# Kernel tuning notes

Hardware: AMD Instinct MI355X
Metric: run time of the kernel (lower is better)

Reference implementation:

```python
import jax, jax.numpy as jnp
import numpy as np

B, C, H, W = 8, 192, 64, 64
HEADS = 4


def _conv(x, w, groups=1):
    # NCHW conv, stride 1, SAME padding (matches 1x1 pad=0 and 3x3 pad=1)
    return jax.lax.conv_general_dilated(
        x, w, window_strides=(1, 1), padding='SAME',
        dimension_numbers=('NCHW', 'OIHW', 'NCHW'),
        feature_group_count=groups)


def setup_inputs() -> dict:
    key = jax.random.key(0)
    k1, k2, k3, k4 = jax.random.split(key, 4)
    x = jax.random.normal(k1, (B, C, H, W), dtype=jnp.float32)
    y = jax.random.normal(k2, (B, C, H, W), dtype=jnp.float32)
    # qkv: Conv2d(C, 3C, 1, bias=False) -> weight (3C, C, 1, 1)
    w_qkv = jax.random.normal(k3, (3 * C, C, 1, 1), dtype=jnp.float32) * 0.02
    # qkv_conv: depthwise Conv2d(3C, 3C, 3, padding=1, groups=3C) -> weight (3C, 1, 3, 3)
    w_dw = jax.random.normal(k4, (3 * C, 1, 3, 3), dtype=jnp.float32) * 0.1
    temperature = jnp.ones((1, HEADS, 1, 1), dtype=jnp.float32)
    return {'x': x, 'y': y, 'w_qkv': w_qkv, 'w_dw': w_dw, 'temperature': temperature}


def reference(x, y, w_qkv, w_dw, temperature):
    b, c, h, w = x.shape
    hw = h * w
    dh = c // HEADS

    def qkv(t):
        t = _conv(_conv(t, w_qkv), w_dw, groups=3 * c)  # (b, 3c, h, w)
        q, k, v = jnp.split(t, 3, axis=1)
        rs = lambda a: a.reshape(b, HEADS, dh, hw)
        return rs(q), rs(k), rs(v)

    q, k, v = qkv(x)
    q1, k1, v1 = qkv(y)

    # F.normalize along last dim (eps = 1e-12)
    def nrm(a):
        n = jnp.sqrt(jnp.sum(a * a, axis=-1, keepdims=True))
        return a / jnp.maximum(n, 1e-12)

    q, k, q1, k1 = nrm(q), nrm(k), nrm(q1), nrm(k1)

    # channel attention: (b, heads, dh, dh), temperature broadcasts (1, heads, 1, 1)
    attn = lambda a, bk: jax.nn.softmax(
        jnp.einsum('bhcn,bhdn->bhcd', a, bk) * temperature, axis=-1)

    attn_u = attn(q, k)
    attn_ud = attn(q, k1)
    attn_d = attn(q1, k1)
    attn_du = attn(q1, k)

    mm = lambda A, V: jnp.einsum('bhcd,bhdn->bhcn', A, V)
    cross_feature = (mm(attn_du, v) + mm(attn_ud, v1)).reshape(b, c, h, w)
    self_feature = (mm(attn_u, v) + mm(attn_d, v1)).reshape(b, c, h, w)
    return cross_feature, self_feature
```

## Files before the change

### kernel.cpp

```cpp
#include <hip/hip_runtime.h>

#define CC   192
#define C3   576
#define HH   64
#define WW   64
#define HWP  4096
#define BB   8
#define DH   48
#define QKV_B (C3*HWP)
#define X_B   (CC*HWP)
#define OUT_HALF ((size_t)BB*X_B)

typedef short bf16x8 __attribute__((ext_vector_type(8)));
typedef float f32x4  __attribute__((ext_vector_type(4)));

#define AS1(p) ((__attribute__((address_space(1))) void*)(p))
#define AS3(p) ((__attribute__((address_space(3))) void*)(p))

__device__ __forceinline__ ushort f2bf(float v) {
    union { float f; unsigned u; } a; a.f = v;
    unsigned r = a.u + 0x7FFF + ((a.u >> 16) & 1);
    return (ushort)(r >> 16);
}
__device__ __forceinline__ float bf2f(ushort h) {
    union { float f; unsigned u; } a; a.u = ((unsigned)h) << 16; return a.f;
}

__global__ __launch_bounds__(256) void convert_single_kernel(const float* __restrict__ in,
    ushort* __restrict__ xt)
{
    __shared__ float L[64][65];
    const int n0 = blockIdx.x * 64, c0 = blockIdx.y * 64, b = blockIdx.z;
    const int t = threadIdx.x;
    const float* ip = in + (size_t)b * X_B;
    #pragma unroll
    for (int i = 0; i < 16; i++) {
        int e = t + 256 * i;
        int r = e >> 6, col = e & 63;
        L[r][col] = ip[(size_t)(c0 + r) * HWP + n0 + col];
    }
    __syncthreads();
    #pragma unroll
    for (int i = 0; i < 4; i++) {
        int e = t + 256 * i;
        int n = e >> 4, c4 = e & 15;
        ushort hi[4];
        #pragma unroll
        for (int j = 0; j < 4; j++)
            hi[j] = f2bf(L[c4 * 4 + j][n]);
        size_t base = ((size_t)(b * HWP + n0 + n)) * 192 + c0 + c4 * 4;
        *(ushort4*)&xt[base] = make_ushort4(hi[0], hi[1], hi[2], hi[3]);
    }
}

__global__ __launch_bounds__(256) void vtrans_kernel(const ushort* __restrict__ in,
    ushort* __restrict__ vt)
{
    __shared__ __align__(16) ushort L[64][72];
    const int n0 = blockIdx.x * 64, c0 = blockIdx.y * 64, b = blockIdx.z;
    const int t = threadIdx.x;
    const ushort* ip = in + (size_t)b * X_B;
    #pragma unroll
    for (int i = 0; i < 2; i++) {
        int e = t + 256 * i;
        int r = e >> 3, u8 = e & 7;
        *(bf16x8*)&L[r][u8 * 8] = *(const bf16x8*)&ip[(size_t)(c0 + r) * HWP + n0 + u8 * 8];
    }
    __syncthreads();
    #pragma unroll
    for (int i = 0; i < 4; i++) {
        int e = t + 256 * i;
        int n = e >> 4, c4 = e & 15;
        ushort o[4];
        #pragma unroll
        for (int j = 0; j < 4; j++) o[j] = L[c4 * 4 + j][n];
        *(ushort4*)&vt[((size_t)(b * HWP + n0 + n)) * 192 + c0 + c4 * 4] =
            make_ushort4(o[0], o[1], o[2], o[3]);
    }
}

__global__ __launch_bounds__(256) void wconvert_kernel(const float* __restrict__ wq,
    ushort* __restrict__ wc)
{
    int e = (blockIdx.x * 256 + threadIdx.x) * 4;
    int oc = e / 192, k = e % 192;
    ushort o[4] = {0, 0, 0, 0};
    if (oc < C3) {
        #pragma unroll
        for (int j = 0; j < 4; j++)
            o[j] = f2bf(wq[oc * CC + k + j]);
    }
    *(ushort4*)&wc[e] = make_ushort4(o[0], o[1], o[2], o[3]);
}

__global__ __launch_bounds__(256) void conv1x1_mfma(const ushort* __restrict__ XT,
    const ushort* __restrict__ Wc, ushort* __restrict__ t1s)
{
    __shared__ __align__(16) ushort Sall[4][128 * 32];
    const int t = threadIdx.x;
    const int lane = t & 63, w = t >> 6;
    const int wm = w >> 1, wn = w & 1;
    const int fr = lane & 15, kg = lane >> 4;
    const int g = blockIdx.x;
    const int xcd = g & 7, s = g >> 3;
    const int bg = xcd;
    const int nt = s / 5;
    const int mi = s % 5;
    const int n0 = nt * 128;
    const int m0 = mi * 128;

    f32x4 acc[4][4] = {};

    auto STAGE = [&](int buf, int ck) {
        const int k0 = ck * 32;
        #pragma unroll
        for (int i = 0; i < 2; i++) {
            int u = i * 256 + w * 64 + lane;
            int rp = u >> 3;
            int p = (u & 7) ^ (rp & 7);
            int r = (rp << 1) | (p >> 2);
            int c = p & 3;
            const ushort* gwh = Wc + (size_t)(m0 + r) * 192 + k0 + c * 8;
            __builtin_amdgcn_global_load_lds(AS1(gwh), AS3(&Sall[buf][(i * 256 + w * 64) * 8]), 16, 0, 0);
            const ushort* gx = XT + ((size_t)(bg * HWP + n0 + r)) * 192 + k0 + c * 8;
            __builtin_amdgcn_global_load_lds(AS1(gx), AS3(&Sall[2 + buf][(i * 256 + w * 64) * 8]), 16, 0, 0);
        }
    };

    STAGE(0, 0);
    __syncthreads();
    int cur = 0;
    for (int ck = 0; ck < 6; ck++) {
        if (ck < 5) STAGE(cur ^ 1, ck + 1);
        bf16x8 afh[4], bfr[4];
        #pragma unroll
        for (int m = 0; m < 4; m++) {
            int R = wm * 64 + m * 16 + fr;
            int unit = (R >> 1) * 8 + ((((R & 1) << 2) | kg) ^ ((R >> 1) & 7));
            afh[m] = *(const bf16x8*)&Sall[cur][unit * 8];
        }
        #pragma unroll
        for (int n = 0; n < 4; n++) {
            int R = wn * 64 + n * 16 + fr;
            int unit = (R >> 1) * 8 + ((((R & 1) << 2) | kg) ^ ((R >> 1) & 7));
            bfr[n] = *(const bf16x8*)&Sall[2 + cur][unit * 8];
        }
        #pragma unroll
        for (int m = 0; m < 4; m++)
            #pragma unroll
            for (int n = 0; n < 4; n++)
                acc[m][n] = __builtin_amdgcn_mfma_f32_16x16x32_bf16(afh[m], bfr[n], acc[m][n], 0, 0, 0);
        __syncthreads();
        cur ^= 1;
    }

    ushort (*E)[128] = (ushort(*)[128])Sall;
    #pragma unroll
    for (int m = 0; m < 4; m++) {
        int rl = wm * 64 + m * 16 + kg * 4;
        #pragma unroll
        for (int n = 0; n < 4; n++) {
            int cl = wn * 64 + n * 16 + fr;
            #pragma unroll
            for (int r = 0; r < 4; r++)
                E[rl + r][cl] = f2bf(acc[m][n][r]);
        }
    }
    __syncthreads();
    ushort* ob = t1s + (size_t)bg * QKV_B;
    #pragma unroll
    for (int i = 0; i < 8; i++) {
        int u = t + 256 * i;
        int row = u >> 4, c8 = u & 15;
        int oc = m0 + row;
        if (oc < C3)
            *(bf16x8*)&ob[(size_t)oc * HWP + n0 + c8 * 8] = *(bf16x8*)&E[row][c8 * 8];
    }
}

__global__ __launch_bounds__(256) void dw3x3_kernel(const ushort* __restrict__ inp,
    const float* __restrict__ wd,
    ushort* __restrict__ qh, ushort* __restrict__ vv, float* __restrict__ inv)
{
    __shared__ float P[66][72];
    const int bc = blockIdx.x;
    const int b = bc / C3, ch = bc % C3;
    const int t = threadIdx.x;
    const ushort* ip = inp + (size_t)bc * HWP;
    float wr[9];
    #pragma unroll
    for (int k = 0; k < 9; k++) wr[k] = wd[ch * 9 + k];
    for (int i = t; i < 66 * 72; i += 256) ((float*)P)[i] = 0.f;
    __syncthreads();
    #pragma unroll
    for (int i = 0; i < 2; i++) {
        int u = t + 256 * i;
        int y = u >> 3, x0 = (u & 7) * 8;
        bf16x8 v8 = *(const bf16x8*)&ip[u * 8];
        #pragma unroll
        for (int j = 0; j < 8; j++)
            P[1 + y][4 + x0 + j] = bf2f((ushort)v8[j]);
    }
    __syncthreads();

    float ssum = 0.f;
    #pragma unroll
    for (int i = 0; i < 4; i++) {
        int u = t + 256 * i;
        int y0 = u >> 4;
        int x0 = (u & 15) * 4;
        float res[4] = {0.f, 0.f, 0.f, 0.f};
        #pragma unroll
        for (int dy = 0; dy < 3; dy++) {
            float4 A = *(float4*)&P[y0 + dy][x0];
            float4 Bv = *(float4*)&P[y0 + dy][x0 + 4];
            float4 Cv = *(float4*)&P[y0 + dy][x0 + 8];
            float c0 = A.w, c1 = Bv.x, c2 = Bv.y, c3 = Bv.z, c4 = Bv.w, c5 = Cv.x;
            float w0 = wr[dy*3], w1 = wr[dy*3+1], w2 = wr[dy*3+2];
            res[0] += w0*c0 + w1*c1 + w2*c2;
            res[1] += w0*c1 + w1*c2 + w2*c3;
            res[2] += w0*c2 + w1*c3 + w2*c4;
            res[3] += w0*c3 + w1*c4 + w2*c5;
        }
        #pragma unroll
        for (int k = 0; k < 4; k++) ssum += res[k] * res[k];
        if (ch < 384) {
            size_t base = ((size_t)b * 384 + ch) * HWP + u * 4;
            *(ushort4*)&qh[base] = make_ushort4(f2bf(res[0]), f2bf(res[1]),
                                                f2bf(res[2]), f2bf(res[3]));
        } else {
            size_t base = ((size_t)b * CC + (ch - 384)) * HWP + u * 4;
            *(ushort4*)&vv[base] = make_ushort4(f2bf(res[0]), f2bf(res[1]),
                                                f2bf(res[2]), f2bf(res[3]));
        }
    }
    if (ch < 384) {
        #pragma unroll
        for (int off = 32; off > 0; off >>= 1) ssum += __shfl_down(ssum, off);
        __shared__ float red[4];
        if ((t & 63) == 0) red[t >> 6] = ssum;
        __syncthreads();
        if (t == 0) {
            float tot = red[0] + red[1] + red[2] + red[3];
            inv[b * 384 + ch] = 1.f / fmaxf(sqrtf(tot), 1e-12f);
        }
    }
}

__global__ __launch_bounds__(256) void gram_mfma(const ushort* __restrict__ qhx,
    const ushort* __restrict__ qhy, float* __restrict__ spart)
{
    __shared__ __align__(16) ushort As[96 * 64];
    __shared__ __align__(16) ushort Bs[96 * 64];
    const int chunk = blockIdx.x, bh = blockIdx.y;
    const int b = bh >> 2, h = bh & 3;
    const int t = threadIdx.x;
    const int lane = t & 63, w = t >> 6;
    const int wm = w >> 1, wn = w & 1;
    const int fr = lane & 15, kg = lane >> 4;

    const size_t qbase = ((size_t)b * 384 + h * DH) * HWP;
    const size_t kbase = ((size_t)b * 384 + 192 + h * DH) * HWP;

    f32x4 acc[3][3] = {};

    for (int ks = 0; ks < 8; ks++) {
        const int n0 = chunk * 512 + ks * 64;
        #pragma unroll
        for (int i = 0; i < 3; i++) {
            int u = i * 256 + w * 64 + lane;
            int r = u >> 3, c = u & 7;
            int cs = c ^ (r & 7);
            const ushort* ga = ((r < DH) ? (qhx + qbase + (size_t)r * HWP)
                                         : (qhy + qbase + (size_t)(r - DH) * HWP))
                               + n0 + cs * 8;
            __builtin_amdgcn_global_load_lds(AS1(ga), AS3(&As[(size_t)(i * 4 + w) * 512]), 16, 0, 0);
            const ushort* gb = ((r < DH) ? (qhx + kbase + (size_t)r * HWP)
                                         : (qhy + kbase + (size_t)(r - DH) * HWP))
                               + n0 + cs * 8;
            __builtin_amdgcn_global_load_lds(AS1(gb), AS3(&Bs[(size_t)(i * 4 + w) * 512]), 16, 0, 0);
        }
        __syncthreads();
        #pragma unroll
        for (int kq = 0; kq < 8; kq += 4) {
            bf16x8 af[3], bfr[3];
            #pragma unroll
            for (int m = 0; m < 3; m++) {
                int R = wm * DH + m * 16 + fr;
                int unit = R * 8 + ((kq + kg) ^ (R & 7));
                af[m] = *(const bf16x8*)&As[unit * 8];
            }
            #pragma unroll
            for (int n = 0; n < 3; n++) {
                int R = wn * DH + n * 16 + fr;
                int unit = R * 8 + ((kq + kg) ^ (R & 7));
                bfr[n] = *(const bf16x8*)&Bs[unit * 8];
            }
            #pragma unroll
            for (int m = 0; m < 3; m++)
                #pragma unroll
                for (int n = 0; n < 3; n++)
                    acc[m][n] = __builtin_amdgcn_mfma_f32_16x16x32_bf16(af[m], bfr[n], acc[m][n], 0, 0, 0);
        }
        __syncthreads();
    }

    float* sp = spart + ((size_t)chunk * 32 + bh) * 9216;
    #pragma unroll
    for (int m = 0; m < 3; m++) {
        int row = wm * DH + m * 16 + kg * 4;
        #pragma unroll
        for (int n = 0; n < 3; n++) {
            int col = wn * DH + n * 16 + fr;
            #pragma unroll
            for (int r = 0; r < 4; r++)
                sp[(row + r) * 96 + col] = acc[m][n][r];
        }
    }
}

__global__ __launch_bounds__(256) void softmax_kernel(const float* __restrict__ spart,
    const float* __restrict__ invx, const float* __restrict__ invy,
    const float* __restrict__ temp, ushort* __restrict__ mpp)
{
    __shared__ float G[96][97];
    const int bh = blockIdx.x, b = bh >> 2, h = bh & 3;
    const int t = threadIdx.x;
    const float ts = temp[h];
    for (int i = 0; i < 36; i++) {
        int f = t + 256 * i;
        float s = 0.f;
        #pragma unroll
        for (int cch = 0; cch < 8; cch++)
            s += spart[((size_t)cch * 32 + bh) * 9216 + f];
        int r = f / 96, c = f % 96;
        float iq = (r < DH) ? invx[b*384 + h*DH + r] : invy[b*384 + h*DH + (r-DH)];
        float ik = (c < DH) ? invx[b*384 + CC + h*DH + c] : invy[b*384 + CC + h*DH + (c-DH)];
        G[r][c] = s * iq * ik * ts;
    }
    __syncthreads();
    if (t < 192) {
        int r = t >> 1, hf = t & 1;
        float* rowp = &G[r][hf * DH];
        float m = rowp[0];
        for (int i = 1; i < DH; i++) m = fmaxf(m, rowp[i]);
        float s = 0.f;
        for (int i = 0; i < DH; i++) { float e = __expf(rowp[i] - m); rowp[i] = e; s += e; }
        float inv = 1.f / s;
        for (int i = 0; i < DH; i++) rowp[i] *= inv;
    }
    __syncthreads();
    ushort* mo = mpp + (size_t)bh * 96 * 128;
    for (int i = 0; i < 12; i++) {
        int f = t + 256 * i;
        int r = f / 32, p = f % 32;
        int ch = p >> 4, j = p & 15;
        mo[(size_t)r * 128 + ch * 64 + 48 + j] = 0;
    }
    for (int i = 0; i < 36; i++) {
        int f = t + 256 * i;
        int r = f / 96, c = f % 96;
        float v;
        if (c < DH) v = (r < DH) ? G[DH + r][c] : G[r - DH][c];
        else        v = G[r][c];
        ushort hi = f2bf(v);
        if (c < DH) mo[(size_t)r * 128 + c] = hi;
        else        mo[(size_t)r * 128 + 64 + (c - DH)] = hi;
    }
}

__global__ __launch_bounds__(256) void outmm_mfma(const ushort* __restrict__ VTx,
    const ushort* __restrict__ VTy, const ushort* __restrict__ mpp,
    float* __restrict__ out)
{
    __shared__ __align__(16) ushort As[96 * 64];
    __shared__ __align__(16) ushort Bs[128 * 64];
    const int t = threadIdx.x;
    const int lane = t & 63, w = t >> 6;
    const int wm = w >> 1, wn = w & 1;
    const int fr = lane & 15, kg = lane >> 4;
    const int nc = blockIdx.x, bh = blockIdx.y;
    const int b = bh >> 2, h = bh & 3;
    const int n0 = nc * 128;
    const ushort* mp = mpp + (size_t)bh * 96 * 128;

    f32x4 acc[3][4] = {};

    for (int kc = 0; kc < 2; kc++) {
        const ushort* Vsrc = kc ? VTy : VTx;
        const int coff = h * DH;
        const int aoff = kc * 64;
        #pragma unroll
        for (int i = 0; i < 3; i++) {
            int u = i * 256 + w * 64 + lane;
            int r = u >> 3, c = u & 7;
            int cs = c ^ (r & 7);
            const ushort* ga = mp + (size_t)r * 128 + aoff + cs * 8;
            __builtin_amdgcn_global_load_lds(AS1(ga), AS3(&As[(size_t)(i * 4 + w) * 512]), 16, 0, 0);
        }
        #pragma unroll
        for (int i = 0; i < 4; i++) {
            int u = i * 256 + w * 64 + lane;
            int r = u >> 3, c = u & 7;
            int cs = c ^ (r & 7);
            int c8 = coff + cs * 8;
            if (c8 >= 192) c8 -= 192;
            const ushort* gb = Vsrc + ((size_t)(b * HWP + n0 + r)) * 192 + c8;
            __builtin_amdgcn_global_load_lds(AS1(gb), AS3(&Bs[(size_t)(i * 4 + w) * 512]), 16, 0, 0);
        }
        __syncthreads();
        #pragma unroll
        for (int kq = 0; kq < 8; kq += 4) {
            bf16x8 af[3], bfr[4];
            #pragma unroll
            for (int m = 0; m < 3; m++) {
                int R = wm * DH + m * 16 + fr;
                int unit = R * 8 + ((kq + kg) ^ (R & 7));
                af[m] = *(const bf16x8*)&As[unit * 8];
            }
            #pragma unroll
            for (int n = 0; n < 4; n++) {
                int R = wn * 64 + n * 16 + fr;
                int unit = R * 8 + ((kq + kg) ^ (R & 7));
                bfr[n] = *(const bf16x8*)&Bs[unit * 8];
            }
            #pragma unroll
            for (int m = 0; m < 3; m++)
                #pragma unroll
                for (int n = 0; n < 4; n++)
                    acc[m][n] = __builtin_amdgcn_mfma_f32_16x16x32_bf16(af[m], bfr[n], acc[m][n], 0, 0, 0);
        }
        __syncthreads();
    }

    #pragma unroll
    for (int m = 0; m < 3; m++) {
        int row = wm * DH + m * 16 + kg * 4;
        #pragma unroll
        for (int n = 0; n < 4; n++) {
            int col = n0 + wn * 64 + n * 16 + fr;
            #pragma unroll
            for (int r = 0; r < 4; r++) {
                int rr = row + r;
                float* dst = (rr < DH)
                    ? (out + (size_t)b * X_B + (h * DH + rr) * HWP + col)
                    : (out + OUT_HALF + (size_t)b * X_B + (h * DH + rr - DH) * HWP + col);
                *dst = acc[m][n][r];
            }
        }
    }
}

extern "C" void kernel_launch(void* const* d_in, const int* in_sizes, int n_in,
                              void* d_out, int out_size, void* d_ws, size_t ws_size,
                              hipStream_t stream)
{
    const float* x  = (const float*)d_in[0];
    const float* y  = (const float*)d_in[1];
    const float* wq = (const float*)d_in[2];
    const float* wd = (const float*)d_in[3];
    const float* tp = (const float*)d_in[4];
    float* out = (float*)d_out;
    float* ws = (float*)d_ws;

    const size_t QKF = 6291456;
    const size_t VBF = 3145728;
    const size_t T1F = 9437184;

    ushort* qhx = (ushort*)(ws);
    ushort* vxs = (ushort*)(ws + QKF);
    ushort* qhy = (ushort*)(ws + QKF + VBF);
    ushort* vys = (ushort*)(ws + 2 * QKF + VBF);
    float*  t1base = ws + 2 * QKF + 2 * VBF;
    ushort* t1s = (ushort*)t1base;
    ushort* XT  = (ushort*)(t1base + T1F);
    ushort* Wc  = (ushort*)(t1base + T1F + VBF);
    float*  invx = t1base + T1F + VBF + 61440;
    float*  invy = invx + 3072;
    ushort* VTx  = t1s;
    ushort* VTy  = (ushort*)(t1base + VBF);
    float*  spart = t1base + 2 * VBF;
    ushort* Mpp  = (ushort*)(t1base + 2 * VBF + 2359296);

    wconvert_kernel<<<120, 256, 0, stream>>>(wq, Wc);

    convert_single_kernel<<<dim3(64, 3, BB), 256, 0, stream>>>(x, XT);
    conv1x1_mfma<<<1280, 256, 0, stream>>>(XT, Wc, t1s);
    dw3x3_kernel<<<BB * C3, 256, 0, stream>>>(t1s, wd, qhx, vxs, invx);

    convert_single_kernel<<<dim3(64, 3, BB), 256, 0, stream>>>(y, XT);
    conv1x1_mfma<<<1280, 256, 0, stream>>>(XT, Wc, t1s);
    dw3x3_kernel<<<BB * C3, 256, 0, stream>>>(t1s, wd, qhy, vys, invy);

    vtrans_kernel<<<dim3(64, 3, BB), 256, 0, stream>>>(vxs, VTx);
    vtrans_kernel<<<dim3(64, 3, BB), 256, 0, stream>>>(vys, VTy);

    gram_mfma<<<dim3(8, 32), 256, 0, stream>>>(qhx, qhy, spart);
    softmax_kernel<<<32, 256, 0, stream>>>(spart, invx, invy, tp, Mpp);
    outmm_mfma<<<dim3(HWP / 128, 32), 256, 0, stream>>>(VTx, VTy, Mpp, out);
}
```

Baseline: 161.3 us.

## Batch x and y through shared convert/conv/dwconv/vtrans launches with wider conv tile

Processes both input tensors in a single launch each for the fp32-to-bf16 transpose, the 1x1 MFMA conv, the depthwise conv and the V transpose, where before there were separate launches per tensor. This halves the number of launches in the front half and gives each launch twice the blocks. The 1x1 conv kernel now uses 512-thread blocks with a 128x256 output tile, staging more X per block and writing the epilogue in two halves through LDS. The workspace layout is reorganised so both tensors' intermediates sit contiguously, which uses more workspace memory.

```diff
diff --git a/kernel.cpp b/kernel.cpp
--- a/kernel.cpp
+++ b/kernel.cpp
@@ -26,13 +26,13 @@
     union { float f; unsigned u; } a; a.u = ((unsigned)h) << 16; return a.f;
 }
 
-__global__ __launch_bounds__(256) void convert_single_kernel(const float* __restrict__ in,
-    ushort* __restrict__ xt)
+__global__ __launch_bounds__(256) void convert_single_kernel(const float* __restrict__ x,
+    const float* __restrict__ y, ushort* __restrict__ xt)
 {
     __shared__ float L[64][65];
-    const int n0 = blockIdx.x * 64, c0 = blockIdx.y * 64, b = blockIdx.z;
-    const int t = threadIdx.x;
-    const float* ip = in + (size_t)b * X_B;
+    const int n0 = blockIdx.x * 64, c0 = blockIdx.y * 64, z = blockIdx.z;
+    const int t = threadIdx.x;
+    const float* ip = ((z < 8) ? x : y) + (size_t)(z & 7) * X_B;
     #pragma unroll
     for (int i = 0; i < 16; i++) {
         int e = t + 256 * i;
@@ -48,7 +48,7 @@
         #pragma unroll
         for (int j = 0; j < 4; j++)
             hi[j] = f2bf(L[c4 * 4 + j][n]);
-        size_t base = ((size_t)(b * HWP + n0 + n)) * 192 + c0 + c4 * 4;
+        size_t base = ((size_t)z * HWP + n0 + n) * 192 + c0 + c4 * 4;
         *(ushort4*)&xt[base] = make_ushort4(hi[0], hi[1], hi[2], hi[3]);
     }
 }
@@ -57,9 +57,9 @@
     ushort* __restrict__ vt)
 {
     __shared__ __align__(16) ushort L[64][72];
-    const int n0 = blockIdx.x * 64, c0 = blockIdx.y * 64, b = blockIdx.z;
-    const int t = threadIdx.x;
-    const ushort* ip = in + (size_t)b * X_B;
+    const int n0 = blockIdx.x * 64, c0 = blockIdx.y * 64, z = blockIdx.z;
+    const int t = threadIdx.x;
+    const ushort* ip = in + (size_t)z * X_B;
     #pragma unroll
     for (int i = 0; i < 2; i++) {
         int e = t + 256 * i;
@@ -74,7 +74,7 @@
         ushort o[4];
         #pragma unroll
         for (int j = 0; j < 4; j++) o[j] = L[c4 * 4 + j][n];
-        *(ushort4*)&vt[((size_t)(b * HWP + n0 + n)) * 192 + c0 + c4 * 4] =
+        *(ushort4*)&vt[((size_t)z * HWP + n0 + n) * 192 + c0 + c4 * 4] =
             make_ushort4(o[0], o[1], o[2], o[3]);
     }
 }
@@ -93,37 +93,48 @@
     *(ushort4*)&wc[e] = make_ushort4(o[0], o[1], o[2], o[3]);
 }
 
-__global__ __launch_bounds__(256) void conv1x1_mfma(const ushort* __restrict__ XT,
+__global__ __launch_bounds__(512) void conv1x1_mfma(const ushort* __restrict__ XT,
     const ushort* __restrict__ Wc, ushort* __restrict__ t1s)
 {
-    __shared__ __align__(16) ushort Sall[4][128 * 32];
+    __shared__ __align__(16) ushort Wsb[2][128 * 32];
+    __shared__ __align__(16) ushort Xsb[2][256 * 32];
     const int t = threadIdx.x;
     const int lane = t & 63, w = t >> 6;
-    const int wm = w >> 1, wn = w & 1;
+    const int wm = w >> 2, wn = w & 3;
     const int fr = lane & 15, kg = lane >> 4;
     const int g = blockIdx.x;
     const int xcd = g & 7, s = g >> 3;
     const int bg = xcd;
-    const int nt = s / 5;
-    const int mi = s % 5;
-    const int n0 = nt * 128;
+    const int tsr = s / 80;
+    const int rem = s - tsr * 80;
+    const int nt = rem / 5;
+    const int mi = rem % 5;
+    const int n0 = nt * 256;
     const int m0 = mi * 128;
+    const ushort* XTp = XT + (size_t)(tsr * 8 + bg) * (HWP * 192);
 
     f32x4 acc[4][4] = {};
 
     auto STAGE = [&](int buf, int ck) {
         const int k0 = ck * 32;
-        #pragma unroll
-        for (int i = 0; i < 2; i++) {
-            int u = i * 256 + w * 64 + lane;
+        {
+            int u = t;
             int rp = u >> 3;
             int p = (u & 7) ^ (rp & 7);
             int r = (rp << 1) | (p >> 2);
             int c = p & 3;
-            const ushort* gwh = Wc + (size_t)(m0 + r) * 192 + k0 + c * 8;
-            __builtin_amdgcn_global_load_lds(AS1(gwh), AS3(&Sall[buf][(i * 256 + w * 64) * 8]), 16, 0, 0);
-            const ushort* gx = XT + ((size_t)(bg * HWP + n0 + r)) * 192 + k0 + c * 8;
-            __builtin_amdgcn_global_load_lds(AS1(gx), AS3(&Sall[2 + buf][(i * 256 + w * 64) * 8]), 16, 0, 0);
+            const ushort* gw = Wc + (size_t)(m0 + r) * 192 + k0 + c * 8;
+            __builtin_amdgcn_global_load_lds(AS1(gw), AS3(&Wsb[buf][(size_t)t * 8]), 16, 0, 0);
+        }
+        #pragma unroll
+        for (int i = 0; i < 2; i++) {
+            int u = i * 512 + t;
+            int rp = u >> 3;
+            int p = (u & 7) ^ (rp & 7);
+            int r = (rp << 1) | (p >> 2);
+            int c = p & 3;
+            const ushort* gx = XTp + (size_t)(n0 + r) * 192 + k0 + c * 8;
+            __builtin_amdgcn_global_load_lds(AS1(gx), AS3(&Xsb[buf][(size_t)(i * 512 + t) * 8]), 16, 0, 0);
         }
     };
 
@@ -137,13 +148,13 @@
         for (int m = 0; m < 4; m++) {
             int R = wm * 64 + m * 16 + fr;
             int unit = (R >> 1) * 8 + ((((R & 1) << 2) | kg) ^ ((R >> 1) & 7));
-            afh[m] = *(const bf16x8*)&Sall[cur][unit * 8];
+            afh[m] = *(const bf16x8*)&Wsb[cur][unit * 8];
         }
         #pragma unroll
         for (int n = 0; n < 4; n++) {
             int R = wn * 64 + n * 16 + fr;
             int unit = (R >> 1) * 8 + ((((R & 1) << 2) | kg) ^ ((R >> 1) & 7));
-            bfr[n] = *(const bf16x8*)&Sall[2 + cur][unit * 8];
+            bfr[n] = *(const bf16x8*)&Xsb[cur][unit * 8];
         }
         #pragma unroll
         for (int m = 0; m < 4; m++)
@@ -154,39 +165,52 @@
         cur ^= 1;
     }
 
-    ushort (*E)[128] = (ushort(*)[128])Sall;
-    #pragma unroll
-    for (int m = 0; m < 4; m++) {
-        int rl = wm * 64 + m * 16 + kg * 4;
-        #pragma unroll
-        for (int n = 0; n < 4; n++) {
-            int cl = wn * 64 + n * 16 + fr;
-            #pragma unroll
-            for (int r = 0; r < 4; r++)
-                E[rl + r][cl] = f2bf(acc[m][n][r]);
-        }
-    }
-    __syncthreads();
-    ushort* ob = t1s + (size_t)bg * QKV_B;
-    #pragma unroll
-    for (int i = 0; i < 8; i++) {
-        int u = t + 256 * i;
-        int row = u >> 4, c8 = u & 15;
-        int oc = m0 + row;
-        if (oc < C3)
-            *(bf16x8*)&ob[(size_t)oc * HWP + n0 + c8 * 8] = *(bf16x8*)&E[row][c8 * 8];
+    ushort (*E)[128] = (ushort(*)[128])Xsb;
+    ushort* ob = t1s + (size_t)tsr * ((size_t)BB * QKV_B) + (size_t)bg * QKV_B;
+    #pragma unroll
+    for (int hf = 0; hf < 2; hf++) {
+        if (hf) __syncthreads();
+        if ((wn >> 1) == hf) {
+            int wn2 = wn & 1;
+            #pragma unroll
+            for (int m = 0; m < 4; m++) {
+                int rl = wm * 64 + m * 16 + kg * 4;
+                #pragma unroll
+                for (int n = 0; n < 4; n++) {
+                    int cl = wn2 * 64 + n * 16 + fr;
+                    #pragma unroll
+                    for (int r = 0; r < 4; r++)
+                        E[rl + r][cl] = f2bf(acc[m][n][r]);
+                }
+            }
+        }
+        __syncthreads();
+        #pragma unroll
+        for (int i = 0; i < 4; i++) {
+            int u = t + 512 * i;
+            int row = u >> 4, c8 = u & 15;
+            int oc = m0 + row;
+            if (oc < C3)
+                *(bf16x8*)&ob[(size_t)oc * HWP + n0 + hf * 128 + c8 * 8] =
+                    *(bf16x8*)&E[row][c8 * 8];
+        }
     }
 }
 
 __global__ __launch_bounds__(256) void dw3x3_kernel(const ushort* __restrict__ inp,
     const float* __restrict__ wd,
-    ushort* __restrict__ qh, ushort* __restrict__ vv, float* __restrict__ inv)
+    ushort* __restrict__ qh0, ushort* __restrict__ vv0, float* __restrict__ inv0)
 {
     __shared__ float P[66][72];
-    const int bc = blockIdx.x;
+    const int bcg = blockIdx.x;
+    const int tsr = bcg / (BB * C3);
+    const int bc = bcg - tsr * (BB * C3);
     const int b = bc / C3, ch = bc % C3;
     const int t = threadIdx.x;
-    const ushort* ip = inp + (size_t)bc * HWP;
+    const ushort* ip = inp + (size_t)tsr * ((size_t)BB * QKV_B) + (size_t)bc * HWP;
+    ushort* qh = qh0 + (size_t)tsr * 12582912;
+    ushort* vv = vv0 + (size_t)tsr * 6291456;
+    float* inv = inv0 + (size_t)tsr * 3072;
     float wr[9];
     #pragma unroll
     for (int k = 0; k < 9; k++) wr[k] = wd[ch * 9 + k];
@@ -463,37 +487,30 @@
     float* out = (float*)d_out;
     float* ws = (float*)d_ws;
 
-    const size_t QKF = 6291456;
-    const size_t VBF = 3145728;
-    const size_t T1F = 9437184;
-
-    ushort* qhx = (ushort*)(ws);
-    ushort* vxs = (ushort*)(ws + QKF);
-    ushort* qhy = (ushort*)(ws + QKF + VBF);
-    ushort* vys = (ushort*)(ws + 2 * QKF + VBF);
-    float*  t1base = ws + 2 * QKF + 2 * VBF;
-    ushort* t1s = (ushort*)t1base;
-    ushort* XT  = (ushort*)(t1base + T1F);
-    ushort* Wc  = (ushort*)(t1base + T1F + VBF);
-    float*  invx = t1base + T1F + VBF + 61440;
-    float*  invy = invx + 3072;
+    ushort* qh0 = (ushort*)ws;
+    float*  v0f = ws + 12582912;
+    ushort* v0  = (ushort*)v0f;
+    float*  t10 = ws + 12582912 + 6291456;
+    ushort* t1s = (ushort*)t10;
+    ushort* XT  = (ushort*)(ws + 12582912 + 6291456 + 18874368);
+    ushort* Wc  = (ushort*)(ws + 12582912 + 6291456 + 18874368 + 6291456);
+    float*  inv0 = ws + 12582912 + 6291456 + 18874368 + 6291456 + 61440;
+    float*  invx = inv0;
+    float*  invy = inv0 + 3072;
     ushort* VTx  = t1s;
-    ushort* VTy  = (ushort*)(t1base + VBF);
-    float*  spart = t1base + 2 * VBF;
-    ushort* Mpp  = (ushort*)(t1base + 2 * VBF + 2359296);
+    ushort* VTy  = (ushort*)(t10 + 3145728);
+    float*  spart = t10 + 6291456;
+    ushort* Mpp  = (ushort*)(t10 + 6291456 + 2359296);
+    ushort* qhx = qh0;
+    ushort* qhy = qh0 + 12582912;
 
     wconvert_kernel<<<120, 256, 0, stream>>>(wq, Wc);
 
-    convert_single_kernel<<<dim3(64, 3, BB), 256, 0, stream>>>(x, XT);
-    conv1x1_mfma<<<1280, 256, 0, stream>>>(XT, Wc, t1s);
-    dw3x3_kernel<<<BB * C3, 256, 0, stream>>>(t1s, wd, qhx, vxs, invx);
-
-    convert_single_kernel<<<dim3(64, 3, BB), 256, 0, stream>>>(y, XT);
-    conv1x1_mfma<<<1280, 256, 0, stream>>>(XT, Wc, t1s);
-    dw3x3_kernel<<<BB * C3, 256, 0, stream>>>(t1s, wd, qhy, vys, invy);
-
-    vtrans_kernel<<<dim3(64, 3, BB), 256, 0, stream>>>(vxs, VTx);
-    vtrans_kernel<<<dim3(64, 3, BB), 256, 0, stream>>>(vys, VTy);
+    convert_single_kernel<<<dim3(64, 3, 16), 256, 0, stream>>>(x, y, XT);
+    conv1x1_mfma<<<1280, 512, 0, stream>>>(XT, Wc, t1s);
+    dw3x3_kernel<<<2 * BB * C3, 256, 0, stream>>>(t1s, wd, qh0, v0, inv0);
+
+    vtrans_kernel<<<dim3(64, 3, 16), 256, 0, stream>>>(v0, VTx);
 
     gram_mfma<<<dim3(8, 32), 256, 0, stream>>>(qhx, qhy, spart);
     softmax_kernel<<<32, 256, 0, stream>>>(spart, invx, invy, tp, Mpp);
```

Result: no change. 158.4 us (-1.8%).
